# Performance work log

Hardware: AMD Instinct MI355X
Metric: run time of the kernel (lower is better)

The kernel has to match this reference:

```python
import jax, jax.numpy as jnp
import numpy as np

N, D, H, DH, FF, NE, NNZ = 4096, 128, 2, 64, 256, 2048, 65536
EPS = 1e-5

def layer_norm(x, g, b):
    m = jnp.mean(x, axis=-1, keepdims=True)
    v = jnp.var(x, axis=-1, keepdims=True)
    return (x - m) / jnp.sqrt(v + EPS) * g + b

def setup_inputs() -> dict:
    key = jax.random.key(0)
    ks = jax.random.split(key, 24)
    s = 0.05
    node_idx = jax.random.randint(ks[1], (NNZ,), 0, N)
    he_idx = jax.random.randint(ks[2], (NNZ,), 0, NE)
    return {
        "x": jax.random.normal(ks[0], (N, D), dtype=jnp.float32),
        "edge": jnp.stack([node_idx, he_idx]).astype(jnp.int64),
        "Wq": jax.random.normal(ks[3], (D, D)) * s, "bq": jnp.zeros((D,)),
        "Wk": jax.random.normal(ks[4], (D, D)) * s, "bk": jnp.zeros((D,)),
        "Wv": jax.random.normal(ks[5], (D, D)) * s, "bv": jnp.zeros((D,)),
        "Wo": jax.random.normal(ks[6], (D, D)) * s, "bo": jnp.zeros((D,)),
        "g_ln1": jnp.ones((D,)), "b_ln1": jnp.zeros((D,)),
        "W1": jax.random.normal(ks[7], (D, FF)) * s, "bf1": jnp.zeros((FF,)),
        "W2": jax.random.normal(ks[8], (FF, D)) * s, "bf2": jnp.zeros((D,)),
        "g_ln2": jnp.ones((D,)), "b_ln2": jnp.zeros((D,)),
        "Wh": jax.random.normal(ks[9], (D, D)) * s, "bh": jnp.zeros((D,)),
    }

def reference(x, edge, Wq, bq, Wk, bk, Wv, bv, Wo, bo, g_ln1, b_ln1,
              W1, bf1, W2, bf2, g_ln2, b_ln2, Wh, bh):
    # dropout layers run in eval mode (identity) for a deterministic reference
    def mha_block(h):
        q = (h @ Wq + bq).reshape(N, H, DH)
        k = (h @ Wk + bk).reshape(N, H, DH)
        v = (h @ Wv + bv).reshape(N, H, DH)
        scores = jnp.einsum('nhd,mhd->hnm', q, k) / jnp.sqrt(jnp.float32(DH))
        attn = jax.nn.softmax(scores, axis=-1)            # [H,N,N]
        o = jnp.einsum('hnm,mhd->nhd', attn, v).reshape(N, D)
        return layer_norm(h + o @ Wo + bo, g_ln1, b_ln1)

    def ff_block(h):
        z = jax.nn.sigmoid(h @ W1 + bf1)
        return layer_norm(h + z @ W2 + bf2, g_ln2, b_ln2)

    h = ff_block(mha_block(x))
    h = ff_block(mha_block(h))

    # HypergraphConv: out = D^{-1} H B^{-1} H^T (X Theta) + bias
    node_idx = edge[0]
    he_idx = edge[1]
    xt = h @ Wh                                            # [N,D]
    ones = jnp.ones((NNZ,), dtype=xt.dtype)
    Bdeg = jax.ops.segment_sum(ones, he_idx, num_segments=NE)
    Binv = jnp.where(Bdeg > 0, 1.0 / Bdeg, 0.0)
    Ddeg = jax.ops.segment_sum(ones, node_idx, num_segments=N)
    Dinv = jnp.where(Ddeg > 0, 1.0 / Ddeg, 0.0)
    e = jax.ops.segment_sum(xt[node_idx], he_idx, num_segments=NE) * Binv[:, None]
    out = jax.ops.segment_sum(e[he_idx], node_idx, num_segments=N) * Dinv[:, None] + bh
    return jax.nn.relu(out)
```

## Files before the change

### kernel.cpp

```cpp
#include <hip/hip_runtime.h>
#include <hip/hip_bf16.h>
#include <cstddef>

#define N_NODES 4096
#define DIM     128
#define NHEAD   2
#define DHEAD   64
#define FFDIM   256
#define NEDGE   2048
#define NNZ_E   65536
#define NSPLIT  8

typedef __attribute__((ext_vector_type(8))) short bf16x8;
typedef __attribute__((ext_vector_type(4))) float f32x4;
typedef unsigned short u16;

__device__ __forceinline__ u16 f2b(float f) {
    unsigned u = __float_as_uint(f);
    return (u16)((u + 0x7FFFu + ((u >> 16) & 1u)) >> 16);
}
__device__ __forceinline__ float b2f_bits(u16 h) {
    return __uint_as_float(((unsigned)h) << 16);
}

__global__ void prep(const float* __restrict__ x, float* __restrict__ h,
                     u16* __restrict__ hh, u16* __restrict__ hl,
                     const float* W0, const float* W1, const float* W2,
                     const float* W3, const float* W4, const float* W5,
                     const float* W6,
                     u16* P0, u16* P1, u16* P2, u16* P3, u16* P4, u16* P5, u16* P6) {
    const int bx = blockIdx.x;
    if (bx < 2048) {
        int i = bx * 256 + threadIdx.x;
        float f = x[i];
        h[i] = f;
        u16 hi = f2b(f);
        hh[i] = hi;
        hl[i] = f2b(f - b2f_bits(hi));
        return;
    }
    const int p = bx - 2048;
    const int sel = p >> 7;
    const float* W; u16* P; int K, NC;
    switch (sel) {
        case 0: W = W0; P = P0; K = 128; NC = 128; break;
        case 1: W = W1; P = P1; K = 128; NC = 128; break;
        case 2: W = W2; P = P2; K = 128; NC = 128; break;
        case 3: W = W3; P = P3; K = 128; NC = 128; break;
        case 4: W = W4; P = P4; K = 128; NC = 128; break;
        case 5: W = W5; P = P5; K = 128; NC = 256; break;
        default: W = W6; P = P6; K = 256; NC = 128; break;
    }
    int i = (p & 127) * 256 + threadIdx.x;
    if (i < K * NC) {
        int k = i / NC, n = i % NC;
        float f = W[i];
        u16 hb = f2b(f);
        size_t o = ((size_t)(k >> 3) * NC + n) * 8 + (k & 7);
        P[o] = hb;
        P[(size_t)K * NC + o] = f2b(f - b2f_bits(hb));
    }
}

template<int K, int NC>
__global__ __launch_bounds__(256) void gemm_mfma(const u16* __restrict__ Ah,
                                                 const u16* __restrict__ Al,
                                                 const u16* __restrict__ Wp,
                                                 float* __restrict__ C0) {
    const int tid = threadIdx.x, w = tid >> 6, lane = tid & 63;
    const int qi = lane & 15, gi = lane >> 4;
    const int row0 = blockIdx.x * 64 + w * 16;
    const int col0 = blockIdx.y * 32;
    const u16* Wlo = Wp + (size_t)K * NC;

    f32x4 acc[2];
    acc[0] = (f32x4){0.f, 0.f, 0.f, 0.f};
    acc[1] = (f32x4){0.f, 0.f, 0.f, 0.f};

#pragma unroll 4
    for (int kc = 0; kc < K / 32; ++kc) {
        const int k0 = kc * 32;
        const size_t ao = (size_t)(row0 + qi) * K + k0 + gi * 8;
        bf16x8 ah = *(const bf16x8*)(Ah + ao);
        bf16x8 al = *(const bf16x8*)(Al + ao);
#pragma unroll
        for (int c = 0; c < 2; ++c) {
            const size_t wo = ((size_t)(k0 / 8 + gi) * NC + col0 + c * 16 + qi) * 8;
            bf16x8 wh = *(const bf16x8*)(Wp + wo);
            bf16x8 wl = *(const bf16x8*)(Wlo + wo);
            acc[c] = __builtin_amdgcn_mfma_f32_16x16x32_bf16(ah, wh, acc[c], 0, 0, 0);
            acc[c] = __builtin_amdgcn_mfma_f32_16x16x32_bf16(al, wh, acc[c], 0, 0, 0);
            acc[c] = __builtin_amdgcn_mfma_f32_16x16x32_bf16(ah, wl, acc[c], 0, 0, 0);
        }
    }

#pragma unroll
    for (int c = 0; c < 2; ++c) {
        const int col = col0 + c * 16 + qi;
#pragma unroll
        for (int r = 0; r < 4; ++r) {
            const int grow = row0 + gi * 4 + r;
            C0[(size_t)grow * NC + col] = acc[c][r];
        }
    }
}

__global__ __launch_bounds__(256) void qkv_mfma(const u16* __restrict__ Ah,
                                                const u16* __restrict__ Al,
                                                const u16* __restrict__ Wq,
                                                const u16* __restrict__ Wk,
                                                const u16* __restrict__ Wv,
                                                const float* __restrict__ bq,
                                                const float* __restrict__ bk,
                                                const float* __restrict__ bv,
                                                u16* __restrict__ qb,
                                                u16* __restrict__ kb,
                                                u16* __restrict__ vtb) {
    const int K = 128, NC = 128;
    const int tid = threadIdx.x, w = tid >> 6, lane = tid & 63;
    const int qi = lane & 15, gi = lane >> 4;
    const int row0 = blockIdx.x * 64 + w * 16;
    const int sel = blockIdx.y >> 2;
    const int col0 = (blockIdx.y & 3) * 32;
    const u16* Wp = (sel == 0) ? Wq : (sel == 1) ? Wk : Wv;
    const float* bias = (sel == 0) ? bq : (sel == 1) ? bk : bv;
    const u16* Wlo = Wp + (size_t)K * NC;

    f32x4 acc[2];
    acc[0] = (f32x4){0.f, 0.f, 0.f, 0.f};
    acc[1] = (f32x4){0.f, 0.f, 0.f, 0.f};

#pragma unroll 4
    for (int kc = 0; kc < K / 32; ++kc) {
        const int k0 = kc * 32;
        const size_t ao = (size_t)(row0 + qi) * K + k0 + gi * 8;
        bf16x8 ah = *(const bf16x8*)(Ah + ao);
        bf16x8 al = *(const bf16x8*)(Al + ao);
#pragma unroll
        for (int c = 0; c < 2; ++c) {
            const size_t wo = ((size_t)(k0 / 8 + gi) * NC + col0 + c * 16 + qi) * 8;
            bf16x8 wh = *(const bf16x8*)(Wp + wo);
            bf16x8 wl = *(const bf16x8*)(Wlo + wo);
            acc[c] = __builtin_amdgcn_mfma_f32_16x16x32_bf16(ah, wh, acc[c], 0, 0, 0);
            acc[c] = __builtin_amdgcn_mfma_f32_16x16x32_bf16(al, wh, acc[c], 0, 0, 0);
            acc[c] = __builtin_amdgcn_mfma_f32_16x16x32_bf16(ah, wl, acc[c], 0, 0, 0);
        }
    }

#pragma unroll
    for (int c = 0; c < 2; ++c) {
        const int col = col0 + c * 16 + qi;
        const int hh = col >> 6, d = col & 63;
        float bv_ = bias[col];
        if (sel < 2) {
            u16* dst = (sel == 0) ? qb : kb;
#pragma unroll
            for (int r = 0; r < 4; ++r) {
                const int grow = row0 + gi * 4 + r;
                dst[((size_t)hh * N_NODES + grow) * 64 + d] = f2b(acc[c][r] + bv_);
            }
        } else {
            const int grow0 = row0 + gi * 4;
            ushort4 pw;
            pw.x = f2b(acc[c][0] + bv_);
            pw.y = f2b(acc[c][1] + bv_);
            pw.z = f2b(acc[c][2] + bv_);
            pw.w = f2b(acc[c][3] + bv_);
            *(ushort4*)&vtb[((size_t)hh * 64 + d) * N_NODES + grow0] = pw;
        }
    }
}

#define ROWP 72
__global__ __launch_bounds__(256) void attn_mfma(const u16* __restrict__ qb,
                                                 const u16* __restrict__ kb,
                                                 const u16* __restrict__ vtb,
                                                 float* __restrict__ op,
                                                 float* __restrict__ mlm,
                                                 float* __restrict__ mll) {
    __shared__ __align__(16) u16 k_s[64 * ROWP];
    __shared__ __align__(16) u16 vt_s[64 * ROWP];
    __shared__ __align__(16) u16 p_s[4][16 * ROWP];
    const int h = blockIdx.y;
    const int s = blockIdx.z;
    const int row0 = blockIdx.x * 64;
    const int tid = threadIdx.x;
    const int w = tid >> 6, lane = tid & 63;
    const int qi = lane & 15, gi = lane >> 4;
    const float CE = 0.18033688011f;

    const u16* qrow = qb + ((size_t)h * N_NODES + row0 + w * 16 + qi) * 64 + gi * 8;
    bf16x8 qf0 = *(const bf16x8*)qrow;
    bf16x8 qf1 = *(const bf16x8*)(qrow + 32);

    f32x4 oc[4];
#pragma unroll
    for (int i = 0; i < 4; ++i) oc[i] = (f32x4){0.f, 0.f, 0.f, 0.f};
    float m_run = -INFINITY, l_run = 0.f;

    const u16* kbh = kb + (size_t)h * N_NODES * 64;
    const u16* vth = vtb + (size_t)h * 64 * N_NODES;

    for (int kt = s * (N_NODES / 64 / NSPLIT); kt < (s + 1) * (N_NODES / 64 / NSPLIT); ++kt) {
        const u16* ksrc = kbh + kt * 64 * 64;
#pragma unroll
        for (int i = 0; i < 2; ++i) {
            int c = tid + i * 256;
            int r = c >> 3, ss = c & 7;
            *(uint4*)&k_s[r * ROWP + ss * 8]  = *(const uint4*)(ksrc + c * 8);
            *(uint4*)&vt_s[r * ROWP + ss * 8] = *(const uint4*)(vth + (size_t)r * N_NODES + kt * 64 + ss * 8);
        }
        __syncthreads();

        f32x4 sc[4];
#pragma unroll
        for (int t = 0; t < 4; ++t) {
            const u16* krow = &k_s[(t * 16 + qi) * ROWP + gi * 8];
            bf16x8 ka0 = *(const bf16x8*)krow;
            bf16x8 ka1 = *(const bf16x8*)(krow + 32);
            f32x4 z = (f32x4){0.f, 0.f, 0.f, 0.f};
            z = __builtin_amdgcn_mfma_f32_16x16x32_bf16(ka0, qf0, z, 0, 0, 0);
            sc[t] = __builtin_amdgcn_mfma_f32_16x16x32_bf16(ka1, qf1, z, 0, 0, 0);
        }

        float smax = -INFINITY;
#pragma unroll
        for (int t = 0; t < 4; ++t)
            smax = fmaxf(smax, fmaxf(fmaxf(sc[t][0], sc[t][1]), fmaxf(sc[t][2], sc[t][3])));
        smax = fmaxf(smax, __shfl_xor(smax, 16));
        smax = fmaxf(smax, __shfl_xor(smax, 32));
        float mn = fmaxf(m_run, smax);
        float alpha = exp2f((m_run - mn) * CE);
        m_run = mn;
        float nb = mn * CE;
        float psum = 0.f;
#pragma unroll
        for (int t = 0; t < 4; ++t) {
            ushort4 pw;
            float p0 = exp2f(fmaf(sc[t][0], CE, -nb)); psum += p0; pw.x = f2b(p0);
            float p1 = exp2f(fmaf(sc[t][1], CE, -nb)); psum += p1; pw.y = f2b(p1);
            float p2 = exp2f(fmaf(sc[t][2], CE, -nb)); psum += p2; pw.z = f2b(p2);
            float p3 = exp2f(fmaf(sc[t][3], CE, -nb)); psum += p3; pw.w = f2b(p3);
            *(ushort4*)&p_s[w][qi * ROWP + t * 16 + gi * 4] = pw;
        }
        psum += __shfl_xor(psum, 16);
        psum += __shfl_xor(psum, 32);
        l_run = l_run * alpha + psum;

        float a0 = __shfl(alpha, gi * 4 + 0);
        float a1 = __shfl(alpha, gi * 4 + 1);
        float a2 = __shfl(alpha, gi * 4 + 2);
        float a3 = __shfl(alpha, gi * 4 + 3);
#pragma unroll
        for (int d = 0; d < 4; ++d) {
            oc[d][0] *= a0; oc[d][1] *= a1; oc[d][2] *= a2; oc[d][3] *= a3;
        }

        const u16* prow = &p_s[w][qi * ROWP];
        bf16x8 pa0 = *(const bf16x8*)(prow + gi * 8);
        bf16x8 pa1 = *(const bf16x8*)(prow + 32 + gi * 8);
#pragma unroll
        for (int d = 0; d < 4; ++d) {
            const u16* vrow = &vt_s[(d * 16 + qi) * ROWP + gi * 8];
            bf16x8 vb0 = *(const bf16x8*)vrow;
            bf16x8 vb1 = *(const bf16x8*)(vrow + 32);
            oc[d] = __builtin_amdgcn_mfma_f32_16x16x32_bf16(pa0, vb0, oc[d], 0, 0, 0);
            oc[d] = __builtin_amdgcn_mfma_f32_16x16x32_bf16(pa1, vb1, oc[d], 0, 0, 0);
        }
        __syncthreads();
    }

    float* opd = op + (size_t)s * N_NODES * 128;
#pragma unroll
    for (int d = 0; d < 4; ++d) {
        size_t cb = h * 64 + d * 16 + qi;
        opd[(size_t)(row0 + w * 16 + gi * 4 + 0) * 128 + cb] = oc[d][0];
        opd[(size_t)(row0 + w * 16 + gi * 4 + 1) * 128 + cb] = oc[d][1];
        opd[(size_t)(row0 + w * 16 + gi * 4 + 2) * 128 + cb] = oc[d][2];
        opd[(size_t)(row0 + w * 16 + gi * 4 + 3) * 128 + cb] = oc[d][3];
    }
    if (gi == 0) {
        size_t mi = (size_t)s * NHEAD * N_NODES + (size_t)h * N_NODES + row0 + w * 16 + qi;
        mlm[mi] = m_run;
        mll[mi] = l_run;
    }
}

#define ROWA 136
__global__ __launch_bounds__(256) void gemm_wo_ln(const float* __restrict__ op,
                                                  const float* __restrict__ mlm,
                                                  const float* __restrict__ mll,
                                                  const u16* __restrict__ Wp,
                                                  const float* __restrict__ bo,
                                                  float* __restrict__ h,
                                                  const float* __restrict__ g,
                                                  const float* __restrict__ b,
                                                  u16* __restrict__ hh,
                                                  u16* __restrict__ hl) {
    const int K = 128, NC = 128;
    __shared__ __align__(16) u16 a_hi[16 * ROWA];
    __shared__ __align__(16) u16 a_lo[16 * ROWA];
    __shared__ float ws_s[NSPLIT][32];
    __shared__ float Linv_s[32];
    __shared__ float wsum[4][16], wsq[4][16];
    const float CE = 0.18033688011f;
    const int tid = threadIdx.x, w = tid >> 6, lane = tid & 63;
    const int qi = lane & 15, gi = lane >> 4;
    const int row0 = blockIdx.x * 16;
    const u16* Wlo = Wp + (size_t)K * NC;

    if (tid < 32) {
        int r = tid >> 1, hd = tid & 1;
        size_t mb = (size_t)hd * N_NODES + row0 + r;
        float m[NSPLIT], l[NSPLIT], mx = -INFINITY;
#pragma unroll
        for (int s = 0; s < NSPLIT; ++s) {
            m[s] = mlm[mb + (size_t)s * NHEAD * N_NODES];
            l[s] = mll[mb + (size_t)s * NHEAD * N_NODES];
            mx = fmaxf(mx, m[s]);
        }
        float L = 0.f;
#pragma unroll
        for (int s = 0; s < NSPLIT; ++s) {
            float ws = exp2f((m[s] - mx) * CE);
            ws_s[s][tid] = ws;
            L += ws * l[s];
        }
        Linv_s[tid] = 1.f / L;
    }
    __syncthreads();

    for (int e = tid; e < 16 * 128; e += 256) {
        int r = e >> 7, c = e & 127, hd = c >> 6;
        size_t idx = (size_t)(row0 + r) * 128 + c;
        float O = 0.f;
#pragma unroll
        for (int s = 0; s < NSPLIT; ++s)
            O += ws_s[s][r * 2 + hd] * op[(size_t)s * N_NODES * 128 + idx];
        float v = O * Linv_s[r * 2 + hd];
        u16 hi = f2b(v);
        a_hi[r * ROWA + c] = hi;
        a_lo[r * ROWA + c] = f2b(v - b2f_bits(hi));
    }
    __syncthreads();

    f32x4 acc[2];
    acc[0] = (f32x4){0.f, 0.f, 0.f, 0.f};
    acc[1] = (f32x4){0.f, 0.f, 0.f, 0.f};
    const int col0 = w * 32;
#pragma unroll
    for (int kc = 0; kc < 4; ++kc) {
        const int k0 = kc * 32;
        bf16x8 ah = *(const bf16x8*)&a_hi[qi * ROWA + k0 + gi * 8];
        bf16x8 al = *(const bf16x8*)&a_lo[qi * ROWA + k0 + gi * 8];
#pragma unroll
        for (int c = 0; c < 2; ++c) {
            const size_t wo = ((size_t)(k0 / 8 + gi) * NC + col0 + c * 16 + qi) * 8;
            bf16x8 wh = *(const bf16x8*)(Wp + wo);
            bf16x8 wl = *(const bf16x8*)(Wlo + wo);
            acc[c] = __builtin_amdgcn_mfma_f32_16x16x32_bf16(ah, wh, acc[c], 0, 0, 0);
            acc[c] = __builtin_amdgcn_mfma_f32_16x16x32_bf16(al, wh, acc[c], 0, 0, 0);
            acc[c] = __builtin_amdgcn_mfma_f32_16x16x32_bf16(ah, wl, acc[c], 0, 0, 0);
        }
    }

    float y[2][4];
    float rs[4], rq[4];
#pragma unroll
    for (int r = 0; r < 4; ++r) { rs[r] = 0.f; rq[r] = 0.f; }
#pragma unroll
    for (int c = 0; c < 2; ++c) {
        const int col = col0 + c * 16 + qi;
        float bv = bo[col];
#pragma unroll
        for (int r = 0; r < 4; ++r) {
            const int grow = row0 + gi * 4 + r;
            float v = acc[c][r] + bv + h[(size_t)grow * 128 + col];
            y[c][r] = v;
            rs[r] += v;
            rq[r] += v * v;
        }
    }
#pragma unroll
    for (int r = 0; r < 4; ++r) {
        for (int msk = 1; msk < 16; msk <<= 1) {
            rs[r] += __shfl_xor(rs[r], msk);
            rq[r] += __shfl_xor(rq[r], msk);
        }
    }
    if (qi == 0) {
#pragma unroll
        for (int r = 0; r < 4; ++r) { wsum[w][gi * 4 + r] = rs[r]; wsq[w][gi * 4 + r] = rq[r]; }
    }
    __syncthreads();
#pragma unroll
    for (int r = 0; r < 4; ++r) {
        const int lr = gi * 4 + r;
        float ts = wsum[0][lr] + wsum[1][lr] + wsum[2][lr] + wsum[3][lr];
        float tq = wsq[0][lr] + wsq[1][lr] + wsq[2][lr] + wsq[3][lr];
        float mean = ts * (1.f / 128.f);
        float var  = tq * (1.f / 128.f) - mean * mean;
        float rstd = rsqrtf(var + 1e-5f);
        const int grow = row0 + lr;
#pragma unroll
        for (int c = 0; c < 2; ++c) {
            const int col = col0 + c * 16 + qi;
            float yn = (y[c][r] - mean) * rstd * g[col] + b[col];
            size_t idx = (size_t)grow * 128 + col;
            h[idx] = yn;
            u16 hi = f2b(yn);
            hh[idx] = hi;
            hl[idx] = f2b(yn - b2f_bits(hi));
        }
    }
}

#define ROWZ 264
__global__ __launch_bounds__(256) void ff_fused(const u16* __restrict__ Ah,
                                                const u16* __restrict__ Al,
                                                const u16* __restrict__ Wp1,
                                                const float* __restrict__ bf1,
                                                const u16* __restrict__ Wp2,
                                                const float* __restrict__ bf2,
                                                float* __restrict__ h,
                                                const float* __restrict__ g,
                                                const float* __restrict__ b,
                                                u16* __restrict__ hh,
                                                u16* __restrict__ hl) {
    __shared__ __align__(16) u16 z_hi[16 * ROWZ];
    __shared__ __align__(16) u16 z_lo[16 * ROWZ];
    __shared__ float wsum[4][16], wsq[4][16];
    const int tid = threadIdx.x, w = tid >> 6, lane = tid & 63;
    const int qi = lane & 15, gi = lane >> 4;
    const int row0 = blockIdx.x * 16;
    const u16* W1lo = Wp1 + (size_t)128 * 256;
    const u16* W2lo = Wp2 + (size_t)256 * 128;

    f32x4 acc1[4];
#pragma unroll
    for (int t = 0; t < 4; ++t) acc1[t] = (f32x4){0.f, 0.f, 0.f, 0.f};
#pragma unroll
    for (int kc = 0; kc < 4; ++kc) {
        const int k0 = kc * 32;
        const size_t ao = (size_t)(row0 + qi) * 128 + k0 + gi * 8;
        bf16x8 ah = *(const bf16x8*)(Ah + ao);
        bf16x8 al = *(const bf16x8*)(Al + ao);
#pragma unroll
        for (int t = 0; t < 4; ++t) {
            const size_t wo = ((size_t)(k0 / 8 + gi) * 256 + w * 64 + t * 16 + qi) * 8;
            bf16x8 wh = *(const bf16x8*)(Wp1 + wo);
            bf16x8 wl = *(const bf16x8*)(W1lo + wo);
            acc1[t] = __builtin_amdgcn_mfma_f32_16x16x32_bf16(ah, wh, acc1[t], 0, 0, 0);
            acc1[t] = __builtin_amdgcn_mfma_f32_16x16x32_bf16(al, wh, acc1[t], 0, 0, 0);
            acc1[t] = __builtin_amdgcn_mfma_f32_16x16x32_bf16(ah, wl, acc1[t], 0, 0, 0);
        }
    }
#pragma unroll
    for (int t = 0; t < 4; ++t) {
        const int col = w * 64 + t * 16 + qi;
        float bv = bf1[col];
#pragma unroll
        for (int r = 0; r < 4; ++r) {
            float v = acc1[t][r] + bv;
            v = 1.f / (1.f + __expf(-v));
            u16 hi = f2b(v);
            const int zr = gi * 4 + r;
            z_hi[zr * ROWZ + col] = hi;
            z_lo[zr * ROWZ + col] = f2b(v - b2f_bits(hi));
        }
    }
    __syncthreads();

    f32x4 acc[2];
    acc[0] = (f32x4){0.f, 0.f, 0.f, 0.f};
    acc[1] = (f32x4){0.f, 0.f, 0.f, 0.f};
    const int col0 = w * 32;
#pragma unroll
    for (int kc = 0; kc < 8; ++kc) {
        const int k0 = kc * 32;
        bf16x8 ah = *(const bf16x8*)&z_hi[qi * ROWZ + k0 + gi * 8];
        bf16x8 al = *(const bf16x8*)&z_lo[qi * ROWZ + k0 + gi * 8];
#pragma unroll
        for (int c = 0; c < 2; ++c) {
            const size_t wo = ((size_t)(k0 / 8 + gi) * 128 + col0 + c * 16 + qi) * 8;
            bf16x8 wh = *(const bf16x8*)(Wp2 + wo);
            bf16x8 wl = *(const bf16x8*)(W2lo + wo);
            acc[c] = __builtin_amdgcn_mfma_f32_16x16x32_bf16(ah, wh, acc[c], 0, 0, 0);
            acc[c] = __builtin_amdgcn_mfma_f32_16x16x32_bf16(al, wh, acc[c], 0, 0, 0);
            acc[c] = __builtin_amdgcn_mfma_f32_16x16x32_bf16(ah, wl, acc[c], 0, 0, 0);
        }
    }

    float y[2][4];
    float rs[4], rq[4];
#pragma unroll
    for (int r = 0; r < 4; ++r) { rs[r] = 0.f; rq[r] = 0.f; }
#pragma unroll
    for (int c = 0; c < 2; ++c) {
        const int col = col0 + c * 16 + qi;
        float bv = bf2[col];
#pragma unroll
        for (int r = 0; r < 4; ++r) {
            const int grow = row0 + gi * 4 + r;
            float v = acc[c][r] + bv + h[(size_t)grow * 128 + col];
            y[c][r] = v;
            rs[r] += v;
            rq[r] += v * v;
        }
    }
#pragma unroll
    for (int r = 0; r < 4; ++r) {
        for (int msk = 1; msk < 16; msk <<= 1) {
            rs[r] += __shfl_xor(rs[r], msk);
            rq[r] += __shfl_xor(rq[r], msk);
        }
    }
    if (qi == 0) {
#pragma unroll
        for (int r = 0; r < 4; ++r) { wsum[w][gi * 4 + r] = rs[r]; wsq[w][gi * 4 + r] = rq[r]; }
    }
    __syncthreads();
#pragma unroll
    for (int r = 0; r < 4; ++r) {
        const int lr = gi * 4 + r;
        float ts = wsum[0][lr] + wsum[1][lr] + wsum[2][lr] + wsum[3][lr];
        float tq = wsq[0][lr] + wsq[1][lr] + wsq[2][lr] + wsq[3][lr];
        float mean = ts * (1.f / 128.f);
        float var  = tq * (1.f / 128.f) - mean * mean;
        float rstd = rsqrtf(var + 1e-5f);
        const int grow = row0 + lr;
#pragma unroll
        for (int c = 0; c < 2; ++c) {
            const int col = col0 + c * 16 + qi;
            float yn = (y[c][r] - mean) * rstd * g[col] + b[col];
            size_t idx = (size_t)grow * 128 + col;
            h[idx] = yn;
            u16 hi = f2b(yn);
            hh[idx] = hi;
            hl[idx] = f2b(yn - b2f_bits(hi));
        }
    }
}

__global__ void hist_kernel(const int* __restrict__ edge_raw,
                            int* __restrict__ nidx, int* __restrict__ hidx,
                            int* __restrict__ cnt_e, int* __restrict__ cnt_n) {
    __shared__ int is64_s;
    if (threadIdx.x < 64) {
        int v = edge_raw[2 * threadIdx.x + 1];
        unsigned long long bal = __ballot(v != 0);
        if (threadIdx.x == 0) is64_s = (bal == 0ull) ? 1 : 0;
    }
    __syncthreads();
    const int is64 = is64_s;
    int i = blockIdx.x * 256 + threadIdx.x;
    if (i < NNZ_E) {
        int ni = (is64 ? edge_raw[2 * i]             : edge_raw[i])         & (N_NODES - 1);
        int he = (is64 ? edge_raw[2 * NNZ_E + 2 * i] : edge_raw[NNZ_E + i]) & (NEDGE - 1);
        nidx[i] = ni;
        hidx[i] = he;
        atomicAdd(&cnt_n[ni], 1);
        atomicAdd(&cnt_e[he], 1);
    }
}

__global__ __launch_bounds__(1024) void scan_only(const int* __restrict__ cnt_e,
                                                  const int* __restrict__ cnt_n,
                                                  int* __restrict__ off_e,
                                                  int* __restrict__ off_n,
                                                  int* __restrict__ cur_e,
                                                  int* __restrict__ cur_n) {
    __shared__ int s[N_NODES];
    const int he_side = (blockIdx.x == 0);
    const int n = he_side ? NEDGE : N_NODES;
    const int* cnt = he_side ? cnt_e : cnt_n;
    int* off = he_side ? off_e : off_n;
    int* cur = he_side ? cur_e : cur_n;
    for (int i = threadIdx.x; i < n; i += 1024) s[i] = cnt[i];
    __syncthreads();
    for (int st = 1; st < n; st <<= 1) {
        int v[4]; int nj = 0;
        for (int i = threadIdx.x; i < n; i += 1024) v[nj++] = (i >= st) ? s[i - st] : 0;
        __syncthreads();
        nj = 0;
        for (int i = threadIdx.x; i < n; i += 1024) s[i] += v[nj++];
        __syncthreads();
    }
    for (int i = threadIdx.x; i < n; i += 1024) { off[i + 1] = s[i]; cur[i] = 0; }
    if (threadIdx.x == 0) off[0] = 0;
}

__global__ void fill_csr(const int* __restrict__ nidx, const int* __restrict__ hidx,
                         const int* __restrict__ off_e, const int* __restrict__ off_n,
                         int* __restrict__ cur_e, int* __restrict__ cur_n,
                         int* __restrict__ csr_e, int* __restrict__ csr_n) {
    int i = blockIdx.x * 256 + threadIdx.x;
    if (i < NNZ_E) {
        int ni = nidx[i], he = hidx[i];
        int p = atomicAdd(&cur_e[he], 1);
        csr_e[off_e[he] + p] = ni;
        int q = atomicAdd(&cur_n[ni], 1);
        csr_n[off_n[ni] + q] = he;
    }
}

__global__ __launch_bounds__(128) void gather_e(const int* __restrict__ off_e,
                                                const int* __restrict__ csr_e,
                                                const float* __restrict__ h,
                                                u16* __restrict__ ehi,
                                                u16* __restrict__ elo) {
    __shared__ int ms[128];
    const int he = blockIdx.x, d = threadIdx.x;
    const int beg = off_e[he], end = off_e[he + 1];
    float acc = 0.f;
    for (int c = beg; c < end; c += 128) {
        int nl = min(128, end - c);
        if (d < nl) ms[d] = csr_e[c + d];
        __syncthreads();
        for (int j = 0; j < nl; ++j) acc += h[(size_t)ms[j] * 128 + d];
        __syncthreads();
    }
    float binv = (end > beg) ? 1.f / (float)(end - beg) : 0.f;
    float v = acc * binv;
    u16 hi = f2b(v);
    ehi[(size_t)he * 128 + d] = hi;
    elo[(size_t)he * 128 + d] = f2b(v - b2f_bits(hi));
}

__global__ __launch_bounds__(128) void gather_n(const int* __restrict__ off_n,
                                                const int* __restrict__ csr_n,
                                                const float* __restrict__ e_sc,
                                                const float* __restrict__ bh,
                                                float* __restrict__ out) {
    __shared__ int ms[128];
    const int nn = blockIdx.x, d = threadIdx.x;
    const int beg = off_n[nn], end = off_n[nn + 1];
    float acc = 0.f;
    for (int c = beg; c < end; c += 128) {
        int nl = min(128, end - c);
        if (d < nl) ms[d] = csr_n[c + d];
        __syncthreads();
        for (int j = 0; j < nl; ++j) acc += e_sc[(size_t)ms[j] * 128 + d];
        __syncthreads();
    }
    float dinv = (end > beg) ? 1.f / (float)(end - beg) : 0.f;
    float v = acc * dinv + bh[d];
    out[(size_t)nn * 128 + d] = v > 0.f ? v : 0.f;
}

extern "C" void kernel_launch(void* const* d_in, const int* in_sizes, int n_in,
                              void* d_out, int out_size, void* d_ws, size_t ws_size,
                              hipStream_t stream) {
    (void)in_sizes; (void)n_in; (void)out_size; (void)ws_size;
    const float* x    = (const float*)d_in[0];
    const int*   edge = (const int*)  d_in[1];
    const float* Wq = (const float*)d_in[2];  const float* bq  = (const float*)d_in[3];
    const float* Wk = (const float*)d_in[4];  const float* bk  = (const float*)d_in[5];
    const float* Wv = (const float*)d_in[6];  const float* bv  = (const float*)d_in[7];
    const float* Wo = (const float*)d_in[8];  const float* bo  = (const float*)d_in[9];
    const float* g1 = (const float*)d_in[10]; const float* b1  = (const float*)d_in[11];
    const float* W1 = (const float*)d_in[12]; const float* bf1 = (const float*)d_in[13];
    const float* W2 = (const float*)d_in[14]; const float* bf2 = (const float*)d_in[15];
    const float* g2 = (const float*)d_in[16]; const float* b2  = (const float*)d_in[17];
    const float* Wh = (const float*)d_in[18]; const float* bh  = (const float*)d_in[19];
    float* out = (float*)d_out;

    float* B = (float*)d_ws;
    float* h    = B;
    u16*   h_hi = (u16*)(B + 524288);
    u16*   h_lo = (u16*)(B + 786432);
    u16*   qb   = (u16*)(B + 1048576);
    u16*   kb   = (u16*)(B + 1310720);
    u16*   vtb  = (u16*)(B + 1835008);
    float* op   = B + 2097152;
    float* mlm  = B + 6291456;
    float* mll  = B + 6356992;
    u16*   e_hi = (u16*)(B + 6946816);
    u16*   e_lo = (u16*)(B + 7077888);
    float* e_sc = B + 7208960;
    u16*   wp_q = (u16*)(B + 8519680);
    u16*   wp_k = (u16*)(B + 8536064);
    u16*   wp_v = (u16*)(B + 8552448);
    u16*   wp_o = (u16*)(B + 8568832);
    u16*   wp_h = (u16*)(B + 8585216);
    u16*   wp_1 = (u16*)(B + 8601600);
    u16*   wp_2 = (u16*)(B + 8634368);
    int*   cur_e = (int*)(B + 9328640);
    int*   cur_n = (int*)(B + 9330688);
    int*   off_e = (int*)(B + 9334784);
    int*   off_n = (int*)(B + 9336840);
    int*   csr_e = (int*)(B + 9340944);
    int*   csr_n = (int*)(B + 9406480);
    int*   cnt_e = (int*)(B + 9472016);
    int*   cnt_n = (int*)(B + 9474064);
    int*   nidx  = (int*)(B + 9478160);
    int*   hidx  = (int*)(B + 9543696);

    prep<<<2048 + 7 * 128, 256, 0, stream>>>(x, h, h_hi, h_lo,
                                             Wq, Wk, Wv, Wo, Wh, W1, W2,
                                             wp_q, wp_k, wp_v, wp_o, wp_h, wp_1, wp_2);

    for (int layer = 0; layer < 2; ++layer) {
        qkv_mfma<<<dim3(64, 12), 256, 0, stream>>>(h_hi, h_lo, wp_q, wp_k, wp_v,
                                                   bq, bk, bv, qb, kb, vtb);
        attn_mfma<<<dim3(N_NODES / 64, NHEAD, NSPLIT), 256, 0, stream>>>(qb, kb, vtb, op, mlm, mll);
        gemm_wo_ln<<<N_NODES / 16, 256, 0, stream>>>(op, mlm, mll, wp_o, bo,
                                                     h, g1, b1, h_hi, h_lo);
        ff_fused<<<N_NODES / 16, 256, 0, stream>>>(h_hi, h_lo, wp_1, bf1, wp_2, bf2,
                                                   h, g2, b2, h_hi, h_lo);
    }

    hipMemsetAsync(cnt_e, 0, (NEDGE + N_NODES) * sizeof(int), stream);
    hist_kernel<<<NNZ_E / 256, 256, 0, stream>>>(edge, nidx, hidx, cnt_e, cnt_n);
    scan_only<<<2, 1024, 0, stream>>>(cnt_e, cnt_n, off_e, off_n, cur_e, cur_n);
    fill_csr<<<NNZ_E / 256, 256, 0, stream>>>(nidx, hidx, off_e, off_n, cur_e, cur_n, csr_e, csr_n);
    gather_e<<<NEDGE, 128, 0, stream>>>(off_e, csr_e, h, e_hi, e_lo);
    gemm_mfma<128, 128><<<dim3(NEDGE / 64, 4), 256, 0, stream>>>(e_hi, e_lo, wp_h, e_sc);
    gather_n<<<N_NODES, 128, 0, stream>>>(off_n, csr_n, e_sc, bh, out);
}
```

Measured before the change: 262.1 us.

## Fuse Wo+LN, FFN+LN and next-layer QKV into one per-layer kernel

Merges gemm_wo_ln, ff_fused and the second layer's QKV projection into a single templated kernel that keeps the intermediate hidden state in shared memory as split bf16 hi/lo plus fp32, so the normalized activations no longer round-trip through global memory between stages. The zeroing of the histogram counters also moves into extra blocks of the prep kernel, replacing the separate memset. Together these drop several kernel launches and global read/write passes. In exchange the fused kernel uses more shared memory per block and has a longer serial chain with more barriers, which may lower occupancy with only 256 blocks.

```diff
diff --git a/kernel.cpp b/kernel.cpp
--- a/kernel.cpp
+++ b/kernel.cpp
@@ -28,7 +28,8 @@
                      const float* W0, const float* W1, const float* W2,
                      const float* W3, const float* W4, const float* W5,
                      const float* W6,
-                     u16* P0, u16* P1, u16* P2, u16* P3, u16* P4, u16* P5, u16* P6) {
+                     u16* P0, u16* P1, u16* P2, u16* P3, u16* P4, u16* P5, u16* P6,
+                     int* __restrict__ cnt) {
     const int bx = blockIdx.x;
     if (bx < 2048) {
         int i = bx * 256 + threadIdx.x;
@@ -37,6 +38,11 @@
         u16 hi = f2b(f);
         hh[i] = hi;
         hl[i] = f2b(f - b2f_bits(hi));
+        return;
+    }
+    if (bx >= 2944) {
+        int i = (bx - 2944) * 256 + threadIdx.x;
+        if (i < NEDGE + N_NODES) cnt[i] = 0;
         return;
     }
     const int p = bx - 2048;
@@ -287,19 +293,27 @@
 }
 
 #define ROWA 136
-__global__ __launch_bounds__(256) void gemm_wo_ln(const float* __restrict__ op,
-                                                  const float* __restrict__ mlm,
-                                                  const float* __restrict__ mll,
-                                                  const u16* __restrict__ Wp,
-                                                  const float* __restrict__ bo,
-                                                  float* __restrict__ h,
-                                                  const float* __restrict__ g,
-                                                  const float* __restrict__ b,
-                                                  u16* __restrict__ hh,
-                                                  u16* __restrict__ hl) {
-    const int K = 128, NC = 128;
-    __shared__ __align__(16) u16 a_hi[16 * ROWA];
-    __shared__ __align__(16) u16 a_lo[16 * ROWA];
+#define ROWZ 264
+#define ROWH 132
+template<int DO_QKV>
+__global__ __launch_bounds__(256) void mega_layer(
+        const float* __restrict__ op, const float* __restrict__ mlm,
+        const float* __restrict__ mll,
+        const u16* __restrict__ wp_o, const float* __restrict__ bo,
+        float* __restrict__ h,
+        const float* __restrict__ g1, const float* __restrict__ b1,
+        const u16* __restrict__ wp_1, const float* __restrict__ bf1,
+        const u16* __restrict__ wp_2, const float* __restrict__ bf2,
+        const float* __restrict__ g2, const float* __restrict__ b2,
+        const u16* __restrict__ wp_q, const u16* __restrict__ wp_k,
+        const u16* __restrict__ wp_v,
+        const float* __restrict__ bq, const float* __restrict__ bk,
+        const float* __restrict__ bv,
+        u16* __restrict__ qb, u16* __restrict__ kb, u16* __restrict__ vtb) {
+    __shared__ __align__(16) u16 zbuf[16 * ROWZ * 2];
+    __shared__ __align__(16) u16 hp_hi[16 * ROWA];
+    __shared__ __align__(16) u16 hp_lo[16 * ROWA];
+    __shared__ float hln[16 * ROWH];
     __shared__ float ws_s[NSPLIT][32];
     __shared__ float Linv_s[32];
     __shared__ float wsum[4][16], wsq[4][16];
@@ -307,7 +321,10 @@
     const int tid = threadIdx.x, w = tid >> 6, lane = tid & 63;
     const int qi = lane & 15, gi = lane >> 4;
     const int row0 = blockIdx.x * 16;
-    const u16* Wlo = Wp + (size_t)K * NC;
+    u16* a_hi = zbuf;
+    u16* a_lo = zbuf + 16 * ROWA;
+    u16* z_hi = zbuf;
+    u16* z_lo = zbuf + 16 * ROWZ;
 
     if (tid < 32) {
         int r = tid >> 1, hd = tid & 1;
@@ -344,200 +361,227 @@
     }
     __syncthreads();
 
-    f32x4 acc[2];
-    acc[0] = (f32x4){0.f, 0.f, 0.f, 0.f};
-    acc[1] = (f32x4){0.f, 0.f, 0.f, 0.f};
-    const int col0 = w * 32;
-#pragma unroll
-    for (int kc = 0; kc < 4; ++kc) {
-        const int k0 = kc * 32;
-        bf16x8 ah = *(const bf16x8*)&a_hi[qi * ROWA + k0 + gi * 8];
-        bf16x8 al = *(const bf16x8*)&a_lo[qi * ROWA + k0 + gi * 8];
-#pragma unroll
-        for (int c = 0; c < 2; ++c) {
-            const size_t wo = ((size_t)(k0 / 8 + gi) * NC + col0 + c * 16 + qi) * 8;
-            bf16x8 wh = *(const bf16x8*)(Wp + wo);
-            bf16x8 wl = *(const bf16x8*)(Wlo + wo);
-            acc[c] = __builtin_amdgcn_mfma_f32_16x16x32_bf16(ah, wh, acc[c], 0, 0, 0);
-            acc[c] = __builtin_amdgcn_mfma_f32_16x16x32_bf16(al, wh, acc[c], 0, 0, 0);
-            acc[c] = __builtin_amdgcn_mfma_f32_16x16x32_bf16(ah, wl, acc[c], 0, 0, 0);
-        }
-    }
-
-    float y[2][4];
-    float rs[4], rq[4];
-#pragma unroll
-    for (int r = 0; r < 4; ++r) { rs[r] = 0.f; rq[r] = 0.f; }
-#pragma unroll
-    for (int c = 0; c < 2; ++c) {
-        const int col = col0 + c * 16 + qi;
-        float bv = bo[col];
-#pragma unroll
-        for (int r = 0; r < 4; ++r) {
-            const int grow = row0 + gi * 4 + r;
-            float v = acc[c][r] + bv + h[(size_t)grow * 128 + col];
-            y[c][r] = v;
-            rs[r] += v;
-            rq[r] += v * v;
-        }
-    }
-#pragma unroll
-    for (int r = 0; r < 4; ++r) {
-        for (int msk = 1; msk < 16; msk <<= 1) {
-            rs[r] += __shfl_xor(rs[r], msk);
-            rq[r] += __shfl_xor(rq[r], msk);
-        }
-    }
-    if (qi == 0) {
-#pragma unroll
-        for (int r = 0; r < 4; ++r) { wsum[w][gi * 4 + r] = rs[r]; wsq[w][gi * 4 + r] = rq[r]; }
-    }
-    __syncthreads();
-#pragma unroll
-    for (int r = 0; r < 4; ++r) {
-        const int lr = gi * 4 + r;
-        float ts = wsum[0][lr] + wsum[1][lr] + wsum[2][lr] + wsum[3][lr];
-        float tq = wsq[0][lr] + wsq[1][lr] + wsq[2][lr] + wsq[3][lr];
-        float mean = ts * (1.f / 128.f);
-        float var  = tq * (1.f / 128.f) - mean * mean;
-        float rstd = rsqrtf(var + 1e-5f);
-        const int grow = row0 + lr;
+    {
+        const u16* Wlo = wp_o + (size_t)128 * 128;
+        f32x4 acc[2];
+        acc[0] = (f32x4){0.f, 0.f, 0.f, 0.f};
+        acc[1] = (f32x4){0.f, 0.f, 0.f, 0.f};
+        const int col0 = w * 32;
+#pragma unroll
+        for (int kc = 0; kc < 4; ++kc) {
+            const int k0 = kc * 32;
+            bf16x8 ah = *(const bf16x8*)&a_hi[qi * ROWA + k0 + gi * 8];
+            bf16x8 al = *(const bf16x8*)&a_lo[qi * ROWA + k0 + gi * 8];
+#pragma unroll
+            for (int c = 0; c < 2; ++c) {
+                const size_t wo = ((size_t)(k0 / 8 + gi) * 128 + col0 + c * 16 + qi) * 8;
+                bf16x8 wh = *(const bf16x8*)(wp_o + wo);
+                bf16x8 wl = *(const bf16x8*)(Wlo + wo);
+                acc[c] = __builtin_amdgcn_mfma_f32_16x16x32_bf16(ah, wh, acc[c], 0, 0, 0);
+                acc[c] = __builtin_amdgcn_mfma_f32_16x16x32_bf16(al, wh, acc[c], 0, 0, 0);
+                acc[c] = __builtin_amdgcn_mfma_f32_16x16x32_bf16(ah, wl, acc[c], 0, 0, 0);
+            }
+        }
+        float y[2][4], rs[4], rq[4];
+#pragma unroll
+        for (int r = 0; r < 4; ++r) { rs[r] = 0.f; rq[r] = 0.f; }
 #pragma unroll
         for (int c = 0; c < 2; ++c) {
             const int col = col0 + c * 16 + qi;
-            float yn = (y[c][r] - mean) * rstd * g[col] + b[col];
-            size_t idx = (size_t)grow * 128 + col;
-            h[idx] = yn;
-            u16 hi = f2b(yn);
-            hh[idx] = hi;
-            hl[idx] = f2b(yn - b2f_bits(hi));
-        }
-    }
-}
-
-#define ROWZ 264
-__global__ __launch_bounds__(256) void ff_fused(const u16* __restrict__ Ah,
-                                                const u16* __restrict__ Al,
-                                                const u16* __restrict__ Wp1,
-                                                const float* __restrict__ bf1,
-                                                const u16* __restrict__ Wp2,
-                                                const float* __restrict__ bf2,
-                                                float* __restrict__ h,
-                                                const float* __restrict__ g,
-                                                const float* __restrict__ b,
-                                                u16* __restrict__ hh,
-                                                u16* __restrict__ hl) {
-    __shared__ __align__(16) u16 z_hi[16 * ROWZ];
-    __shared__ __align__(16) u16 z_lo[16 * ROWZ];
-    __shared__ float wsum[4][16], wsq[4][16];
-    const int tid = threadIdx.x, w = tid >> 6, lane = tid & 63;
-    const int qi = lane & 15, gi = lane >> 4;
-    const int row0 = blockIdx.x * 16;
-    const u16* W1lo = Wp1 + (size_t)128 * 256;
-    const u16* W2lo = Wp2 + (size_t)256 * 128;
-
-    f32x4 acc1[4];
-#pragma unroll
-    for (int t = 0; t < 4; ++t) acc1[t] = (f32x4){0.f, 0.f, 0.f, 0.f};
-#pragma unroll
-    for (int kc = 0; kc < 4; ++kc) {
-        const int k0 = kc * 32;
-        const size_t ao = (size_t)(row0 + qi) * 128 + k0 + gi * 8;
-        bf16x8 ah = *(const bf16x8*)(Ah + ao);
-        bf16x8 al = *(const bf16x8*)(Al + ao);
+            float bv = bo[col];
+#pragma unroll
+            for (int r = 0; r < 4; ++r) {
+                float v = acc[c][r] + bv + h[(size_t)(row0 + gi * 4 + r) * 128 + col];
+                y[c][r] = v;
+                rs[r] += v; rq[r] += v * v;
+            }
+        }
+#pragma unroll
+        for (int r = 0; r < 4; ++r)
+            for (int msk = 1; msk < 16; msk <<= 1) {
+                rs[r] += __shfl_xor(rs[r], msk);
+                rq[r] += __shfl_xor(rq[r], msk);
+            }
+        if (qi == 0) {
+#pragma unroll
+            for (int r = 0; r < 4; ++r) { wsum[w][gi * 4 + r] = rs[r]; wsq[w][gi * 4 + r] = rq[r]; }
+        }
+        __syncthreads();
+#pragma unroll
+        for (int r = 0; r < 4; ++r) {
+            const int lr = gi * 4 + r;
+            float ts = wsum[0][lr] + wsum[1][lr] + wsum[2][lr] + wsum[3][lr];
+            float tq = wsq[0][lr] + wsq[1][lr] + wsq[2][lr] + wsq[3][lr];
+            float mean = ts * (1.f / 128.f);
+            float var  = tq * (1.f / 128.f) - mean * mean;
+            float rstd = rsqrtf(var + 1e-5f);
+#pragma unroll
+            for (int c = 0; c < 2; ++c) {
+                const int col = col0 + c * 16 + qi;
+                float yn = (y[c][r] - mean) * rstd * g1[col] + b1[col];
+                hln[lr * ROWH + col] = yn;
+                u16 hi = f2b(yn);
+                hp_hi[lr * ROWA + col] = hi;
+                hp_lo[lr * ROWA + col] = f2b(yn - b2f_bits(hi));
+            }
+        }
+    }
+    __syncthreads();
+
+    {
+        const u16* W1lo = wp_1 + (size_t)128 * 256;
+        f32x4 acc1[4];
+#pragma unroll
+        for (int t = 0; t < 4; ++t) acc1[t] = (f32x4){0.f, 0.f, 0.f, 0.f};
+#pragma unroll
+        for (int kc = 0; kc < 4; ++kc) {
+            const int k0 = kc * 32;
+            bf16x8 ah = *(const bf16x8*)&hp_hi[qi * ROWA + k0 + gi * 8];
+            bf16x8 al = *(const bf16x8*)&hp_lo[qi * ROWA + k0 + gi * 8];
+#pragma unroll
+            for (int t = 0; t < 4; ++t) {
+                const size_t wo = ((size_t)(k0 / 8 + gi) * 256 + w * 64 + t * 16 + qi) * 8;
+                bf16x8 wh = *(const bf16x8*)(wp_1 + wo);
+                bf16x8 wl = *(const bf16x8*)(W1lo + wo);
+                acc1[t] = __builtin_amdgcn_mfma_f32_16x16x32_bf16(ah, wh, acc1[t], 0, 0, 0);
+                acc1[t] = __builtin_amdgcn_mfma_f32_16x16x32_bf16(al, wh, acc1[t], 0, 0, 0);
+                acc1[t] = __builtin_amdgcn_mfma_f32_16x16x32_bf16(ah, wl, acc1[t], 0, 0, 0);
+            }
+        }
+        __syncthreads();
 #pragma unroll
         for (int t = 0; t < 4; ++t) {
-            const size_t wo = ((size_t)(k0 / 8 + gi) * 256 + w * 64 + t * 16 + qi) * 8;
-            bf16x8 wh = *(const bf16x8*)(Wp1 + wo);
-            bf16x8 wl = *(const bf16x8*)(W1lo + wo);
-            acc1[t] = __builtin_amdgcn_mfma_f32_16x16x32_bf16(ah, wh, acc1[t], 0, 0, 0);
-            acc1[t] = __builtin_amdgcn_mfma_f32_16x16x32_bf16(al, wh, acc1[t], 0, 0, 0);
-            acc1[t] = __builtin_amdgcn_mfma_f32_16x16x32_bf16(ah, wl, acc1[t], 0, 0, 0);
-        }
-    }
-#pragma unroll
-    for (int t = 0; t < 4; ++t) {
-        const int col = w * 64 + t * 16 + qi;
-        float bv = bf1[col];
-#pragma unroll
-        for (int r = 0; r < 4; ++r) {
-            float v = acc1[t][r] + bv;
-            v = 1.f / (1.f + __expf(-v));
-            u16 hi = f2b(v);
-            const int zr = gi * 4 + r;
-            z_hi[zr * ROWZ + col] = hi;
-            z_lo[zr * ROWZ + col] = f2b(v - b2f_bits(hi));
+            const int col = w * 64 + t * 16 + qi;
+            float bv = bf1[col];
+#pragma unroll
+            for (int r = 0; r < 4; ++r) {
+                float v = acc1[t][r] + bv;
+                v = 1.f / (1.f + __expf(-v));
+                u16 hi = f2b(v);
+                const int zr = gi * 4 + r;
+                z_hi[zr * ROWZ + col] = hi;
+                z_lo[zr * ROWZ + col] = f2b(v - b2f_bits(hi));
+            }
         }
     }
     __syncthreads();
 
-    f32x4 acc[2];
-    acc[0] = (f32x4){0.f, 0.f, 0.f, 0.f};
-    acc[1] = (f32x4){0.f, 0.f, 0.f, 0.f};
-    const int col0 = w * 32;
-#pragma unroll
-    for (int kc = 0; kc < 8; ++kc) {
-        const int k0 = kc * 32;
-        bf16x8 ah = *(const bf16x8*)&z_hi[qi * ROWZ + k0 + gi * 8];
-        bf16x8 al = *(const bf16x8*)&z_lo[qi * ROWZ + k0 + gi * 8];
-#pragma unroll
-        for (int c = 0; c < 2; ++c) {
-            const size_t wo = ((size_t)(k0 / 8 + gi) * 128 + col0 + c * 16 + qi) * 8;
-            bf16x8 wh = *(const bf16x8*)(Wp2 + wo);
-            bf16x8 wl = *(const bf16x8*)(W2lo + wo);
-            acc[c] = __builtin_amdgcn_mfma_f32_16x16x32_bf16(ah, wh, acc[c], 0, 0, 0);
-            acc[c] = __builtin_amdgcn_mfma_f32_16x16x32_bf16(al, wh, acc[c], 0, 0, 0);
-            acc[c] = __builtin_amdgcn_mfma_f32_16x16x32_bf16(ah, wl, acc[c], 0, 0, 0);
-        }
-    }
-
-    float y[2][4];
-    float rs[4], rq[4];
-#pragma unroll
-    for (int r = 0; r < 4; ++r) { rs[r] = 0.f; rq[r] = 0.f; }
-#pragma unroll
-    for (int c = 0; c < 2; ++c) {
-        const int col = col0 + c * 16 + qi;
-        float bv = bf2[col];
-#pragma unroll
-        for (int r = 0; r < 4; ++r) {
-            const int grow = row0 + gi * 4 + r;
-            float v = acc[c][r] + bv + h[(size_t)grow * 128 + col];
-            y[c][r] = v;
-            rs[r] += v;
-            rq[r] += v * v;
-        }
-    }
-#pragma unroll
-    for (int r = 0; r < 4; ++r) {
-        for (int msk = 1; msk < 16; msk <<= 1) {
-            rs[r] += __shfl_xor(rs[r], msk);
-            rq[r] += __shfl_xor(rq[r], msk);
-        }
-    }
-    if (qi == 0) {
-#pragma unroll
-        for (int r = 0; r < 4; ++r) { wsum[w][gi * 4 + r] = rs[r]; wsq[w][gi * 4 + r] = rq[r]; }
-    }
-    __syncthreads();
-#pragma unroll
-    for (int r = 0; r < 4; ++r) {
-        const int lr = gi * 4 + r;
-        float ts = wsum[0][lr] + wsum[1][lr] + wsum[2][lr] + wsum[3][lr];
-        float tq = wsq[0][lr] + wsq[1][lr] + wsq[2][lr] + wsq[3][lr];
-        float mean = ts * (1.f / 128.f);
-        float var  = tq * (1.f / 128.f) - mean * mean;
-        float rstd = rsqrtf(var + 1e-5f);
-        const int grow = row0 + lr;
+    {
+        const u16* W2lo = wp_2 + (size_t)256 * 128;
+        f32x4 acc[2];
+        acc[0] = (f32x4){0.f, 0.f, 0.f, 0.f};
+        acc[1] = (f32x4){0.f, 0.f, 0.f, 0.f};
+        const int col0 = w * 32;
+#pragma unroll
+        for (int kc = 0; kc < 8; ++kc) {
+            const int k0 = kc * 32;
+            bf16x8 ah = *(const bf16x8*)&z_hi[qi * ROWZ + k0 + gi * 8];
+            bf16x8 al = *(const bf16x8*)&z_lo[qi * ROWZ + k0 + gi * 8];
+#pragma unroll
+            for (int c = 0; c < 2; ++c) {
+                const size_t wo = ((size_t)(k0 / 8 + gi) * 128 + col0 + c * 16 + qi) * 8;
+                bf16x8 wh = *(const bf16x8*)(wp_2 + wo);
+                bf16x8 wl = *(const bf16x8*)(W2lo + wo);
+                acc[c] = __builtin_amdgcn_mfma_f32_16x16x32_bf16(ah, wh, acc[c], 0, 0, 0);
+                acc[c] = __builtin_amdgcn_mfma_f32_16x16x32_bf16(al, wh, acc[c], 0, 0, 0);
+                acc[c] = __builtin_amdgcn_mfma_f32_16x16x32_bf16(ah, wl, acc[c], 0, 0, 0);
+            }
+        }
+        float y[2][4], rs[4], rq[4];
+#pragma unroll
+        for (int r = 0; r < 4; ++r) { rs[r] = 0.f; rq[r] = 0.f; }
 #pragma unroll
         for (int c = 0; c < 2; ++c) {
             const int col = col0 + c * 16 + qi;
-            float yn = (y[c][r] - mean) * rstd * g[col] + b[col];
-            size_t idx = (size_t)grow * 128 + col;
-            h[idx] = yn;
-            u16 hi = f2b(yn);
-            hh[idx] = hi;
-            hl[idx] = f2b(yn - b2f_bits(hi));
+            float bv = bf2[col];
+#pragma unroll
+            for (int r = 0; r < 4; ++r) {
+                float v = acc[c][r] + bv + hln[(gi * 4 + r) * ROWH + col];
+                y[c][r] = v;
+                rs[r] += v; rq[r] += v * v;
+            }
+        }
+#pragma unroll
+        for (int r = 0; r < 4; ++r)
+            for (int msk = 1; msk < 16; msk <<= 1) {
+                rs[r] += __shfl_xor(rs[r], msk);
+                rq[r] += __shfl_xor(rq[r], msk);
+            }
+        if (qi == 0) {
+#pragma unroll
+            for (int r = 0; r < 4; ++r) { wsum[w][gi * 4 + r] = rs[r]; wsq[w][gi * 4 + r] = rq[r]; }
+        }
+        __syncthreads();
+#pragma unroll
+        for (int r = 0; r < 4; ++r) {
+            const int lr = gi * 4 + r;
+            float ts = wsum[0][lr] + wsum[1][lr] + wsum[2][lr] + wsum[3][lr];
+            float tq = wsq[0][lr] + wsq[1][lr] + wsq[2][lr] + wsq[3][lr];
+            float mean = ts * (1.f / 128.f);
+            float var  = tq * (1.f / 128.f) - mean * mean;
+            float rstd = rsqrtf(var + 1e-5f);
+#pragma unroll
+            for (int c = 0; c < 2; ++c) {
+                const int col = col0 + c * 16 + qi;
+                float yn = (y[c][r] - mean) * rstd * g2[col] + b2[col];
+                h[(size_t)(row0 + lr) * 128 + col] = yn;
+                if (DO_QKV) {
+                    u16 hi = f2b(yn);
+                    hp_hi[lr * ROWA + col] = hi;
+                    hp_lo[lr * ROWA + col] = f2b(yn - b2f_bits(hi));
+                }
+            }
+        }
+    }
+
+    if (DO_QKV) {
+        __syncthreads();
+        const int col0 = w * 32;
+#pragma unroll
+        for (int sel = 0; sel < 3; ++sel) {
+            const u16* Wp = (sel == 0) ? wp_q : (sel == 1) ? wp_k : wp_v;
+            const float* bias = (sel == 0) ? bq : (sel == 1) ? bk : bv;
+            const u16* Wlo = Wp + (size_t)128 * 128;
+            f32x4 acc[2];
+            acc[0] = (f32x4){0.f, 0.f, 0.f, 0.f};
+            acc[1] = (f32x4){0.f, 0.f, 0.f, 0.f};
+#pragma unroll
+            for (int kc = 0; kc < 4; ++kc) {
+                const int k0 = kc * 32;
+                bf16x8 ah = *(const bf16x8*)&hp_hi[qi * ROWA + k0 + gi * 8];
+                bf16x8 al = *(const bf16x8*)&hp_lo[qi * ROWA + k0 + gi * 8];
+#pragma unroll
+                for (int c = 0; c < 2; ++c) {
+                    const size_t wo = ((size_t)(k0 / 8 + gi) * 128 + col0 + c * 16 + qi) * 8;
+                    bf16x8 wh = *(const bf16x8*)(Wp + wo);
+                    bf16x8 wl = *(const bf16x8*)(Wlo + wo);
+                    acc[c] = __builtin_amdgcn_mfma_f32_16x16x32_bf16(ah, wh, acc[c], 0, 0, 0);
+                    acc[c] = __builtin_amdgcn_mfma_f32_16x16x32_bf16(al, wh, acc[c], 0, 0, 0);
+                    acc[c] = __builtin_amdgcn_mfma_f32_16x16x32_bf16(ah, wl, acc[c], 0, 0, 0);
+                }
+            }
+#pragma unroll
+            for (int c = 0; c < 2; ++c) {
+                const int col = col0 + c * 16 + qi;
+                const int hh = col >> 6, d = col & 63;
+                float bv_ = bias[col];
+                if (sel < 2) {
+                    u16* dst = (sel == 0) ? qb : kb;
+#pragma unroll
+                    for (int r = 0; r < 4; ++r) {
+                        const int grow = row0 + gi * 4 + r;
+                        dst[((size_t)hh * N_NODES + grow) * 64 + d] = f2b(acc[c][r] + bv_);
+                    }
+                } else {
+                    const int grow0 = row0 + gi * 4;
+                    ushort4 pw;
+                    pw.x = f2b(acc[c][0] + bv_);
+                    pw.y = f2b(acc[c][1] + bv_);
+                    pw.z = f2b(acc[c][2] + bv_);
+                    pw.w = f2b(acc[c][3] + bv_);
+                    *(ushort4*)&vtb[((size_t)hh * 64 + d) * N_NODES + grow0] = pw;
+                }
+            }
         }
     }
 }
@@ -696,21 +740,24 @@
     int*   nidx  = (int*)(B + 9478160);
     int*   hidx  = (int*)(B + 9543696);
 
-    prep<<<2048 + 7 * 128, 256, 0, stream>>>(x, h, h_hi, h_lo,
-                                             Wq, Wk, Wv, Wo, Wh, W1, W2,
-                                             wp_q, wp_k, wp_v, wp_o, wp_h, wp_1, wp_2);
-
-    for (int layer = 0; layer < 2; ++layer) {
-        qkv_mfma<<<dim3(64, 12), 256, 0, stream>>>(h_hi, h_lo, wp_q, wp_k, wp_v,
-                                                   bq, bk, bv, qb, kb, vtb);
-        attn_mfma<<<dim3(N_NODES / 64, NHEAD, NSPLIT), 256, 0, stream>>>(qb, kb, vtb, op, mlm, mll);
-        gemm_wo_ln<<<N_NODES / 16, 256, 0, stream>>>(op, mlm, mll, wp_o, bo,
-                                                     h, g1, b1, h_hi, h_lo);
-        ff_fused<<<N_NODES / 16, 256, 0, stream>>>(h_hi, h_lo, wp_1, bf1, wp_2, bf2,
-                                                   h, g2, b2, h_hi, h_lo);
-    }
-
-    hipMemsetAsync(cnt_e, 0, (NEDGE + N_NODES) * sizeof(int), stream);
+    prep<<<2968, 256, 0, stream>>>(x, h, h_hi, h_lo,
+                                   Wq, Wk, Wv, Wo, Wh, W1, W2,
+                                   wp_q, wp_k, wp_v, wp_o, wp_h, wp_1, wp_2, cnt_e);
+
+    qkv_mfma<<<dim3(64, 12), 256, 0, stream>>>(h_hi, h_lo, wp_q, wp_k, wp_v,
+                                               bq, bk, bv, qb, kb, vtb);
+    attn_mfma<<<dim3(N_NODES / 64, NHEAD, NSPLIT), 256, 0, stream>>>(qb, kb, vtb, op, mlm, mll);
+    mega_layer<1><<<N_NODES / 16, 256, 0, stream>>>(op, mlm, mll, wp_o, bo, h, g1, b1,
+                                                    wp_1, bf1, wp_2, bf2, g2, b2,
+                                                    wp_q, wp_k, wp_v, bq, bk, bv,
+                                                    qb, kb, vtb);
+    attn_mfma<<<dim3(N_NODES / 64, NHEAD, NSPLIT), 256, 0, stream>>>(qb, kb, vtb, op, mlm, mll);
+    mega_layer<0><<<N_NODES / 16, 256, 0, stream>>>(op, mlm, mll, wp_o, bo, h, g1, b1,
+                                                    wp_1, bf1, wp_2, bf2, g2, b2,
+                                                    nullptr, nullptr, nullptr,
+                                                    nullptr, nullptr, nullptr,
+                                                    nullptr, nullptr, nullptr);
+
     hist_kernel<<<NNZ_E / 256, 256, 0, stream>>>(edge, nidx, hidx, cnt_e, cnt_n);
     scan_only<<<2, 1024, 0, stream>>>(cnt_e, cnt_n, off_e, off_n, cur_e, cur_n);
     fill_csr<<<NNZ_E / 256, 256, 0, stream>>>(nidx, hidx, off_e, off_n, cur_e, cur_n, csr_e, csr_n);
```

Measured after the change: 256.1 us. 1.02x faster.
